# Kernel tuning notes

Hardware: AMD Instinct MI355X
Metric: run time of the kernel (lower is better)

Reference implementation:

```python
import jax, jax.numpy as jnp
import numpy as np

B, NW, L, D = 32, 64, 49, 192
HEADS, PROJ = 8, 256
HD = PROJ // HEADS  # 32


def setup_inputs() -> dict:
    key = jax.random.key(0)
    ks = jax.random.split(key, 12)
    s = 0.02
    return {
        "query": jax.random.normal(ks[0], (B, NW, L, D), jnp.float32),
        "key_": jax.random.normal(ks[1], (B, NW, L, D), jnp.float32),
        "value": jax.random.normal(ks[2], (B, NW, L, D), jnp.float32),
        "mask": jax.random.randint(ks[3], (1, NW, 1, L, L), 0, 2).astype(bool),
        "Wq": jax.random.normal(ks[4], (D, PROJ), jnp.float32) * s,
        "bq": jnp.zeros((PROJ,), jnp.float32),
        "Wk": jax.random.normal(ks[5], (D, PROJ), jnp.float32) * s,
        "bk": jnp.zeros((PROJ,), jnp.float32),
        "Wv": jax.random.normal(ks[6], (D, PROJ), jnp.float32) * s,
        "Ww": jax.random.normal(ks[7], (PROJ, D), jnp.float32) * s,
        "bw": jnp.zeros((D,), jnp.float32),
    }


def reference(query, key_, value, mask, Wq, bq, Wk, bk, Wv, Ww, bw):
    scale = 1.0 / (HD ** 0.5)
    # projections, split heads: [B, NW, L, PROJ] -> [B, NW, H, L, HD]
    def split_heads(x):
        return x.reshape(B, NW, L, HEADS, HD).transpose(0, 1, 3, 2, 4)

    q = split_heads(query @ Wq + bq)
    k = split_heads(key_ @ Wk + bk)
    v = split_heads(value @ Wv)  # no bias, matching proj_v

    # scores: [B, NW, H, L, L]
    scores = jnp.einsum("bwhnc,bwhmc->bwhnm", q, k) * scale
    scores = jnp.where(mask, jnp.float32(-1000.0), scores)
    attn = jax.nn.softmax(scores, axis=-1)
    # dropout inactive: training=False and enable_sampling=False

    out = jnp.einsum("bwhnm,bwhmc->bwhnc", attn, v)
    out = out.transpose(0, 1, 3, 2, 4).reshape(B, NW, L, PROJ)
    out = out @ Ww + bw
    return out
```

## Files before the change

### kernel.cpp

```cpp
#include <hip/hip_runtime.h>

#define B_    32
#define NW_   64
#define BW_   2048
#define L_    49
#define D_    192
#define PROJ_ 256
#define H_    8
#define HD_   32

typedef __attribute__((ext_vector_type(8))) short bf16x8;
typedef __attribute__((ext_vector_type(4))) float f32x4;

#define QK_OFF    24576
#define LDS_BYTES 78848

__device__ __forceinline__ short f2bf(float f) {
    union { float f; unsigned u; } v; v.f = f;
    unsigned r = v.u + 0x7FFFu + ((v.u >> 16) & 1u);
    return (short)(r >> 16);
}

__device__ __forceinline__ unsigned cvtpk(float lo, float hi) {
    unsigned r;
    asm("v_cvt_pk_bf16_f32 %0, %1, %2" : "=v"(r) : "v"(lo), "v"(hi));
    return r;
}

__global__ __launch_bounds__(256) void prep_kernel(
    const float* __restrict__ Wq, const float* __restrict__ Wk,
    const float* __restrict__ Wv, const float* __restrict__ Ww,
    const int* __restrict__ mask,
    short* __restrict__ Wqt, short* __restrict__ Wkt,
    short* __restrict__ Wvt, short* __restrict__ Wwt,
    unsigned long long* __restrict__ mbits)
{
    const int b   = blockIdx.x;
    const int tid = threadIdx.x;
    if (b < 768) {
        const int sel = b >> 8, n = b & 255;
        const float* src = (sel == 0) ? Wq : (sel == 1) ? Wk : Wv;
        short* dst = (sel == 0) ? Wqt : (sel == 1) ? Wkt : Wvt;
        if (tid < D_) dst[n * D_ + tid] = f2bf(src[tid * PROJ_ + n]);
    } else if (b < 960) {
        const int n = b - 768;
        Wwt[n * PROJ_ + tid] = f2bf(Ww[tid * D_ + n]);
    } else {
        const int m = b - 960;
        const int w = m >> 2, chunk = m & 3;
        const int wave = tid >> 6, lane = tid & 63;
        #pragma unroll
        for (int k = 0; k < 4; ++k) {
            const int q = chunk * 16 + wave * 4 + k;
            int val = 0;
            if (q < L_ && lane < L_) val = mask[w * (L_ * L_) + q * L_ + lane];
            unsigned long long bits = __ballot(val != 0);
            if (lane == 0) mbits[w * 64 + q] = bits;
        }
    }
}

__global__ __launch_bounds__(256, 2) void fused_kernel(
    const float* __restrict__ query, const float* __restrict__ key_,
    const float* __restrict__ value,
    const short* __restrict__ Wqt, const short* __restrict__ Wkt,
    const short* __restrict__ Wvt,
    const float* __restrict__ bq, const float* __restrict__ bk,
    const unsigned long long* __restrict__ mbits,
    const short* __restrict__ Wwt, const float* __restrict__ bwb,
    float* __restrict__ out)
{
    extern __shared__ char lds[];

    const int bw   = blockIdx.x;
    const int w    = bw & (NW_ - 1);
    const int tid  = threadIdx.x;
    const int wave = tid >> 6;
    const int lane = tid & 63;
    const int m16  = lane & 15;
    const int quad = lane >> 4;

    const int swz2 = ((m16 >> 1) & 3) << 4;
    const int swz3 = (m16 & 7) << 4;

    char* qkR  = lds + QK_OFF;
    char* slot = lds + wave * 4096;

    unsigned long long mb[4];
    #pragma unroll
    for (int nt = 0; nt < 4; ++nt) mb[nt] = mbits[w * 64 + nt * 16 + m16];

    uint2 vpk[2][4];

    #pragma unroll
    for (int sel = 0; sel < 3; ++sel) {
        const float* x  = (sel == 0) ? query : (sel == 1) ? key_ : value;
        const short* Wt = (sel == 0) ? Wqt : (sel == 1) ? Wkt : Wvt;

        __syncthreads();
        #pragma unroll
        for (int it = 0; it < 12; ++it) {
            const int i = tid + it * 256;
            const int l = i / 48, c4 = i - l * 48;
            uint2 u = {0u, 0u};
            if (l < L_) {
                float4 v = *(const float4*)&x[((size_t)bw * L_ + l) * D_ + c4 * 4];
                u.x = cvtpk(v.x, v.y); u.y = cvtpk(v.z, v.w);
            }
            *(uint2*)(lds + l * 384 + ((c4 * 8) ^ ((l & 7) << 4))) = u;
        }
        __syncthreads();

        f32x4 acc[4][4];
        #pragma unroll
        for (int mt = 0; mt < 4; ++mt)
            #pragma unroll
            for (int nt = 0; nt < 4; ++nt)
                acc[mt][nt] = (f32x4){0.f, 0.f, 0.f, 0.f};

        #pragma unroll
        for (int kc = 0; kc < 6; ++kc) {
            bf16x8 af[4], bfr[4];
            #pragma unroll
            for (int mt = 0; mt < 4; ++mt)
                af[mt] = *(const bf16x8*)(lds + (mt * 16 + m16) * 384 +
                                          ((kc * 64 + quad * 16) ^ swz3));
            #pragma unroll
            for (int nt = 0; nt < 4; ++nt)
                bfr[nt] = *(const bf16x8*)&Wt[(size_t)(wave * 64 + nt * 16 + m16) * D_ +
                                              kc * 32 + quad * 8];
            __builtin_amdgcn_s_setprio(1);
            #pragma unroll
            for (int mt = 0; mt < 4; ++mt)
                #pragma unroll
                for (int nt = 0; nt < 4; ++nt)
                    acc[mt][nt] = __builtin_amdgcn_mfma_f32_16x16x32_bf16(
                        af[mt], bfr[nt], acc[mt][nt], 0, 0, 0);
            __builtin_amdgcn_s_setprio(0);
        }

        if (sel == 2) __syncthreads();

        if (sel < 2) {
            const float* bsel = (sel == 0) ? bq : bk;
            #pragma unroll
            for (int nt = 0; nt < 4; ++nt) {
                const int head = wave * 2 + (nt >> 1);
                const int c = (nt & 1) * 16 + m16;
                const float bias = bsel[wave * 64 + nt * 16 + m16];
                char* db = qkR + head * 6272 + sel * 3136;
                #pragma unroll
                for (int mt = 0; mt < 4; ++mt)
                    #pragma unroll
                    for (int r = 0; r < 4; ++r) {
                        const int i = mt * 16 + quad * 4 + r;
                        if (i < L_)
                            *(short*)(db + i * 64 + ((2 * c) ^ (((i >> 1) & 3) << 4))) =
                                f2bf(acc[mt][nt][r] + bias);
                    }
            }
        } else {
            #pragma unroll
            for (int nt = 0; nt < 4; ++nt) {
                const int c = (nt & 1) * 16 + m16;
                #pragma unroll
                for (int mt = 0; mt < 4; ++mt) {
                    uint2 p;
                    p.x = cvtpk(acc[mt][nt][0], acc[mt][nt][1]);
                    p.y = cvtpk(acc[mt][nt][2], acc[mt][nt][3]);
                    if (nt < 2)
                        *(uint2*)(slot + c * 128 + ((mt * 32 + quad * 8) ^ swz3)) = p;
                    else
                        vpk[nt - 2][mt] = p;
                }
            }
        }
    }

    const float scale = 0.17677669529663687f;

    #pragma unroll 1
    for (int hh = 0; hh < 2; ++hh) {
        const int head = wave * 2 + hh;
        char* qb = qkR + head * 6272;
        char* kb = qb + 3136;

        f32x4 sacc[4][4];
        #pragma unroll
        for (int mt = 0; mt < 4; ++mt)
            #pragma unroll
            for (int nt = 0; nt < 4; ++nt)
                sacc[mt][nt] = (f32x4){0.f, 0.f, 0.f, 0.f};
        {
            bf16x8 kf[4], qf[4];
            #pragma unroll
            for (int mt = 0; mt < 4; ++mt)
                kf[mt] = *(const bf16x8*)(kb + (mt * 16 + m16) * 64 + ((quad * 16) ^ swz2));
            #pragma unroll
            for (int nt = 0; nt < 4; ++nt)
                qf[nt] = *(const bf16x8*)(qb + (nt * 16 + m16) * 64 + ((quad * 16) ^ swz2));
            __builtin_amdgcn_s_setprio(1);
            #pragma unroll
            for (int mt = 0; mt < 4; ++mt)
                #pragma unroll
                for (int nt = 0; nt < 4; ++nt)
                    sacc[mt][nt] = __builtin_amdgcn_mfma_f32_16x16x32_bf16(
                        kf[mt], qf[nt], sacc[mt][nt], 0, 0, 0);
            __builtin_amdgcn_s_setprio(0);
        }

        #pragma unroll
        for (int nt = 0; nt < 4; ++nt) {
            float e[4][4];
            float mx = -1e30f;
            #pragma unroll
            for (int mt = 0; mt < 4; ++mt)
                #pragma unroll
                for (int r = 0; r < 4; ++r) {
                    const int k = mt * 16 + quad * 4 + r;
                    float v = sacc[mt][nt][r] * scale;
                    if (k >= L_) v = -INFINITY;
                    else if ((mb[nt] >> k) & 1ull) v = -1000.0f;
                    e[mt][r] = v;
                    mx = fmaxf(mx, v);
                }
            mx = fmaxf(mx, __shfl_xor(mx, 16, 64));
            mx = fmaxf(mx, __shfl_xor(mx, 32, 64));
            float sum = 0.f;
            #pragma unroll
            for (int mt = 0; mt < 4; ++mt)
                #pragma unroll
                for (int r = 0; r < 4; ++r) {
                    const float ev = __expf(e[mt][r] - mx);
                    e[mt][r] = ev;
                    sum += ev;
                }
            sum += __shfl_xor(sum, 16, 64);
            sum += __shfl_xor(sum, 32, 64);
            const float inv = 1.0f / sum;
            const int prow = nt * 16 + m16;
            if (prow < L_) {
                #pragma unroll
                for (int mt = 0; mt < 4; ++mt) {
                    uint2 p;
                    p.x = cvtpk(e[mt][0] * inv, e[mt][1] * inv);
                    p.y = cvtpk(e[mt][2] * inv, e[mt][3] * inv);
                    *(uint2*)(qb + prow * 128 + ((mt * 32 + quad * 8) ^ swz3)) = p;
                }
            }
        }

        f32x4 oacc[2][4];
        #pragma unroll
        for (int mt2 = 0; mt2 < 2; ++mt2)
            #pragma unroll
            for (int nt = 0; nt < 4; ++nt)
                oacc[mt2][nt] = (f32x4){0.f, 0.f, 0.f, 0.f};
        #pragma unroll
        for (int kc = 0; kc < 2; ++kc) {
            bf16x8 vf[2], pf[4];
            #pragma unroll
            for (int mt2 = 0; mt2 < 2; ++mt2)
                vf[mt2] = *(const bf16x8*)(slot + (mt2 * 16 + m16) * 128 +
                                           ((kc * 64 + quad * 16) ^ swz3));
            #pragma unroll
            for (int nt = 0; nt < 4; ++nt)
                pf[nt] = *(const bf16x8*)(qb + (nt * 16 + m16) * 128 +
                                          ((kc * 64 + quad * 16) ^ swz3));
            __builtin_amdgcn_s_setprio(1);
            #pragma unroll
            for (int mt2 = 0; mt2 < 2; ++mt2)
                #pragma unroll
                for (int nt = 0; nt < 4; ++nt)
                    oacc[mt2][nt] = __builtin_amdgcn_mfma_f32_16x16x32_bf16(
                        vf[mt2], pf[nt], oacc[mt2][nt], 0, 0, 0);
            __builtin_amdgcn_s_setprio(0);
        }

        #pragma unroll
        for (int nt = 0; nt < 4; ++nt) {
            const int prow = nt * 16 + m16;
            if (prow < L_) {
                #pragma unroll
                for (int mt2 = 0; mt2 < 2; ++mt2) {
                    uint2 o;
                    o.x = cvtpk(oacc[mt2][nt][0], oacc[mt2][nt][1]);
                    o.y = cvtpk(oacc[mt2][nt][2], oacc[mt2][nt][3]);
                    *(uint2*)(qb + prow * 64 +
                              ((mt2 * 32 + quad * 8) ^ (((prow >> 1) & 3) << 4))) = o;
                }
            }
        }

        if (hh == 0) {
            #pragma unroll
            for (int nt2 = 0; nt2 < 2; ++nt2) {
                const int c = nt2 * 16 + m16;
                #pragma unroll
                for (int mt = 0; mt < 4; ++mt)
                    *(uint2*)(slot + c * 128 + ((mt * 32 + quad * 8) ^ swz3)) = vpk[nt2][mt];
            }
        }
    }

    __syncthreads();

    f32x4 cacc[4][3];
    #pragma unroll
    for (int mt = 0; mt < 4; ++mt)
        #pragma unroll
        for (int nt = 0; nt < 3; ++nt)
            cacc[mt][nt] = (f32x4){0.f, 0.f, 0.f, 0.f};
    #pragma unroll
    for (int kc = 0; kc < 8; ++kc) {
        char* Oh = qkR + kc * 6272;
        bf16x8 af[4], bfw[3];
        #pragma unroll
        for (int mt = 0; mt < 4; ++mt)
            af[mt] = *(const bf16x8*)(Oh + (mt * 16 + m16) * 64 + ((quad * 16) ^ swz2));
        #pragma unroll
        for (int nt = 0; nt < 3; ++nt)
            bfw[nt] = *(const bf16x8*)&Wwt[(size_t)(wave * 48 + nt * 16 + m16) * PROJ_ +
                                           kc * 32 + quad * 8];
        __builtin_amdgcn_s_setprio(1);
        #pragma unroll
        for (int mt = 0; mt < 4; ++mt)
            #pragma unroll
            for (int nt = 0; nt < 3; ++nt)
                cacc[mt][nt] = __builtin_amdgcn_mfma_f32_16x16x32_bf16(
                    af[mt], bfw[nt], cacc[mt][nt], 0, 0, 0);
        __builtin_amdgcn_s_setprio(0);
    }
    #pragma unroll
    for (int nt = 0; nt < 3; ++nt) {
        const int col = wave * 48 + nt * 16 + m16;
        const float bias = bwb[col];
        #pragma unroll
        for (int mt = 0; mt < 4; ++mt)
            #pragma unroll
            for (int r = 0; r < 4; ++r) {
                const int i = mt * 16 + quad * 4 + r;
                if (i < L_)
                    out[((size_t)bw * L_ + i) * D_ + col] = cacc[mt][nt][r] + bias;
            }
    }
}

extern "C" void kernel_launch(void* const* d_in, const int* in_sizes, int n_in,
                              void* d_out, int out_size, void* d_ws, size_t ws_size,
                              hipStream_t stream) {
    const float* query = (const float*)d_in[0];
    const float* key_  = (const float*)d_in[1];
    const float* value = (const float*)d_in[2];
    const int*   mask  = (const int*)d_in[3];
    const float* Wq    = (const float*)d_in[4];
    const float* bq    = (const float*)d_in[5];
    const float* Wk    = (const float*)d_in[6];
    const float* bk    = (const float*)d_in[7];
    const float* Wv    = (const float*)d_in[8];
    const float* Ww    = (const float*)d_in[9];
    const float* bw    = (const float*)d_in[10];
    float* out = (float*)d_out;

    unsigned long long* mbits = (unsigned long long*)d_ws;
    short* Wqt = (short*)(mbits + 64 * 64);
    short* Wkt = Wqt + PROJ_ * D_;
    short* Wvt = Wkt + PROJ_ * D_;
    short* Wwt = Wvt + PROJ_ * D_;

    static bool attr_set = false;
    if (!attr_set) {
        (void)hipFuncSetAttribute(reinterpret_cast<const void*>(fused_kernel),
                                  hipFuncAttributeMaxDynamicSharedMemorySize, LDS_BYTES);
        attr_set = true;
    }

    prep_kernel<<<dim3(1216), 256, 0, stream>>>(Wq, Wk, Wv, Ww, mask,
                                                Wqt, Wkt, Wvt, Wwt, mbits);
    fused_kernel<<<dim3(BW_), 256, LDS_BYTES, stream>>>(
        query, key_, value, Wqt, Wkt, Wvt, bq, bk, mbits, Wwt, bw, out);
}
```

Before: 367.0 us.

## Use 8 waves per block with one head per wave and in-kernel mask bits

Doubles the block to 512 threads so each wave owns a single attention head instead of two. The Q/K/V projection and output-projection work is split across twice as many waves, and V staging is compacted to make room. Mask bit-packing moves from the prep kernel into the fused kernel's LDS, removing the mbits workspace. This trades more waves per block and higher register pressure under launch_bounds(512,4), and adds a per-block mask read, against shorter serial per-wave work and more latency hiding.

```diff
diff --git a/kernel.cpp b/kernel.cpp
--- a/kernel.cpp
+++ b/kernel.cpp
@@ -13,7 +13,8 @@
 typedef __attribute__((ext_vector_type(4))) float f32x4;
 
 #define QK_OFF    24576
-#define LDS_BYTES 78848
+#define MROW_OFF  74752
+#define LDS_BYTES 76800
 
 __device__ __forceinline__ short f2bf(float f) {
     union { float f; unsigned u; } v; v.f = f;
@@ -27,13 +28,11 @@
     return r;
 }
 
-__global__ __launch_bounds__(256) void prep_kernel(
+__global__ __launch_bounds__(256) void prep_weights(
     const float* __restrict__ Wq, const float* __restrict__ Wk,
     const float* __restrict__ Wv, const float* __restrict__ Ww,
-    const int* __restrict__ mask,
     short* __restrict__ Wqt, short* __restrict__ Wkt,
-    short* __restrict__ Wvt, short* __restrict__ Wwt,
-    unsigned long long* __restrict__ mbits)
+    short* __restrict__ Wvt, short* __restrict__ Wwt)
 {
     const int b   = blockIdx.x;
     const int tid = threadIdx.x;
@@ -42,31 +41,19 @@
         const float* src = (sel == 0) ? Wq : (sel == 1) ? Wk : Wv;
         short* dst = (sel == 0) ? Wqt : (sel == 1) ? Wkt : Wvt;
         if (tid < D_) dst[n * D_ + tid] = f2bf(src[tid * PROJ_ + n]);
-    } else if (b < 960) {
+    } else {
         const int n = b - 768;
         Wwt[n * PROJ_ + tid] = f2bf(Ww[tid * D_ + n]);
-    } else {
-        const int m = b - 960;
-        const int w = m >> 2, chunk = m & 3;
-        const int wave = tid >> 6, lane = tid & 63;
-        #pragma unroll
-        for (int k = 0; k < 4; ++k) {
-            const int q = chunk * 16 + wave * 4 + k;
-            int val = 0;
-            if (q < L_ && lane < L_) val = mask[w * (L_ * L_) + q * L_ + lane];
-            unsigned long long bits = __ballot(val != 0);
-            if (lane == 0) mbits[w * 64 + q] = bits;
-        }
-    }
-}
-
-__global__ __launch_bounds__(256, 2) void fused_kernel(
+    }
+}
+
+__global__ __launch_bounds__(512, 4) void fused_kernel(
     const float* __restrict__ query, const float* __restrict__ key_,
     const float* __restrict__ value,
     const short* __restrict__ Wqt, const short* __restrict__ Wkt,
     const short* __restrict__ Wvt,
     const float* __restrict__ bq, const float* __restrict__ bk,
-    const unsigned long long* __restrict__ mbits,
+    const int* __restrict__ mask,
     const short* __restrict__ Wwt, const float* __restrict__ bwb,
     float* __restrict__ out)
 {
@@ -83,12 +70,10 @@
     const int swz2 = ((m16 >> 1) & 3) << 4;
     const int swz3 = (m16 & 7) << 4;
 
-    char* qkR  = lds + QK_OFF;
-    char* slot = lds + wave * 4096;
-
-    unsigned long long mb[4];
-    #pragma unroll
-    for (int nt = 0; nt < 4; ++nt) mb[nt] = mbits[w * 64 + nt * 16 + m16];
+    char* qb = lds + QK_OFF + wave * 6272;
+    char* kb = qb + 3136;
+    char* vslot = lds + wave * 2560;
+    unsigned long long* mrow = (unsigned long long*)(lds + MROW_OFF);
 
     uint2 vpk[2][4];
 
@@ -99,8 +84,8 @@
 
         __syncthreads();
         #pragma unroll
-        for (int it = 0; it < 12; ++it) {
-            const int i = tid + it * 256;
+        for (int it = 0; it < 6; ++it) {
+            const int i = tid + it * 512;
             const int l = i / 48, c4 = i - l * 48;
             uint2 u = {0u, 0u};
             if (l < L_) {
@@ -109,46 +94,54 @@
             }
             *(uint2*)(lds + l * 384 + ((c4 * 8) ^ ((l & 7) << 4))) = u;
         }
+        if (sel == 0) {
+            #pragma unroll
+            for (int rr = 0; rr < 8; ++rr) {
+                const int row = wave * 8 + rr;
+                int val = 0;
+                if (row < L_ && lane < L_)
+                    val = mask[w * (L_ * L_) + row * L_ + lane];
+                unsigned long long bits = __ballot(val != 0);
+                if (lane == 0) mrow[row] = bits;
+            }
+        }
         __syncthreads();
 
-        f32x4 acc[4][4];
-        #pragma unroll
-        for (int mt = 0; mt < 4; ++mt)
-            #pragma unroll
-            for (int nt = 0; nt < 4; ++nt)
+        f32x4 acc[4][2];
+        #pragma unroll
+        for (int mt = 0; mt < 4; ++mt)
+            #pragma unroll
+            for (int nt = 0; nt < 2; ++nt)
                 acc[mt][nt] = (f32x4){0.f, 0.f, 0.f, 0.f};
 
         #pragma unroll
         for (int kc = 0; kc < 6; ++kc) {
-            bf16x8 af[4], bfr[4];
+            bf16x8 af[4], bfr[2];
             #pragma unroll
             for (int mt = 0; mt < 4; ++mt)
                 af[mt] = *(const bf16x8*)(lds + (mt * 16 + m16) * 384 +
                                           ((kc * 64 + quad * 16) ^ swz3));
             #pragma unroll
-            for (int nt = 0; nt < 4; ++nt)
-                bfr[nt] = *(const bf16x8*)&Wt[(size_t)(wave * 64 + nt * 16 + m16) * D_ +
+            for (int nt = 0; nt < 2; ++nt)
+                bfr[nt] = *(const bf16x8*)&Wt[(size_t)(wave * 32 + nt * 16 + m16) * D_ +
                                               kc * 32 + quad * 8];
             __builtin_amdgcn_s_setprio(1);
             #pragma unroll
             for (int mt = 0; mt < 4; ++mt)
                 #pragma unroll
-                for (int nt = 0; nt < 4; ++nt)
+                for (int nt = 0; nt < 2; ++nt)
                     acc[mt][nt] = __builtin_amdgcn_mfma_f32_16x16x32_bf16(
                         af[mt], bfr[nt], acc[mt][nt], 0, 0, 0);
             __builtin_amdgcn_s_setprio(0);
         }
 
-        if (sel == 2) __syncthreads();
-
         if (sel < 2) {
             const float* bsel = (sel == 0) ? bq : bk;
-            #pragma unroll
-            for (int nt = 0; nt < 4; ++nt) {
-                const int head = wave * 2 + (nt >> 1);
-                const int c = (nt & 1) * 16 + m16;
-                const float bias = bsel[wave * 64 + nt * 16 + m16];
-                char* db = qkR + head * 6272 + sel * 3136;
+            char* db = (sel == 0) ? qb : kb;
+            #pragma unroll
+            for (int nt = 0; nt < 2; ++nt) {
+                const int c = nt * 16 + m16;
+                const float bias = bsel[wave * 32 + c];
                 #pragma unroll
                 for (int mt = 0; mt < 4; ++mt)
                     #pragma unroll
@@ -161,188 +154,188 @@
             }
         } else {
             #pragma unroll
-            for (int nt = 0; nt < 4; ++nt) {
-                const int c = (nt & 1) * 16 + m16;
+            for (int nt = 0; nt < 2; ++nt)
                 #pragma unroll
                 for (int mt = 0; mt < 4; ++mt) {
-                    uint2 p;
-                    p.x = cvtpk(acc[mt][nt][0], acc[mt][nt][1]);
-                    p.y = cvtpk(acc[mt][nt][2], acc[mt][nt][3]);
-                    if (nt < 2)
-                        *(uint2*)(slot + c * 128 + ((mt * 32 + quad * 8) ^ swz3)) = p;
-                    else
-                        vpk[nt - 2][mt] = p;
+                    vpk[nt][mt].x = cvtpk(acc[mt][nt][0], acc[mt][nt][1]);
+                    vpk[nt][mt].y = cvtpk(acc[mt][nt][2], acc[mt][nt][3]);
                 }
-            }
-        }
-    }
+        }
+    }
+
+    __syncthreads();
+
+    #pragma unroll
+    for (int nt = 0; nt < 2; ++nt)
+        #pragma unroll
+        for (int mt = 0; mt < 2; ++mt)
+            *(uint2*)(vslot + (nt * 16 + m16) * 80 + mt * 32 + quad * 8) = vpk[nt][mt];
+
+    unsigned long long mb[4];
+    #pragma unroll
+    for (int nt = 0; nt < 4; ++nt) mb[nt] = mrow[nt * 16 + m16];
 
     const float scale = 0.17677669529663687f;
 
-    #pragma unroll 1
-    for (int hh = 0; hh < 2; ++hh) {
-        const int head = wave * 2 + hh;
-        char* qb = qkR + head * 6272;
-        char* kb = qb + 3136;
-
-        f32x4 sacc[4][4];
+    f32x4 sacc[4][4];
+    #pragma unroll
+    for (int mt = 0; mt < 4; ++mt)
+        #pragma unroll
+        for (int nt = 0; nt < 4; ++nt)
+            sacc[mt][nt] = (f32x4){0.f, 0.f, 0.f, 0.f};
+    {
+        bf16x8 kf[4], qf[4];
+        #pragma unroll
+        for (int mt = 0; mt < 4; ++mt)
+            kf[mt] = *(const bf16x8*)(kb + (mt * 16 + m16) * 64 + ((quad * 16) ^ swz2));
+        #pragma unroll
+        for (int nt = 0; nt < 4; ++nt)
+            qf[nt] = *(const bf16x8*)(qb + (nt * 16 + m16) * 64 + ((quad * 16) ^ swz2));
+        __builtin_amdgcn_s_setprio(1);
         #pragma unroll
         for (int mt = 0; mt < 4; ++mt)
             #pragma unroll
             for (int nt = 0; nt < 4; ++nt)
-                sacc[mt][nt] = (f32x4){0.f, 0.f, 0.f, 0.f};
-        {
-            bf16x8 kf[4], qf[4];
+                sacc[mt][nt] = __builtin_amdgcn_mfma_f32_16x16x32_bf16(
+                    kf[mt], qf[nt], sacc[mt][nt], 0, 0, 0);
+        __builtin_amdgcn_s_setprio(0);
+    }
+
+    #pragma unroll
+    for (int nt = 0; nt < 4; ++nt) {
+        float e[4][4];
+        float mx = -1e30f;
+        #pragma unroll
+        for (int mt = 0; mt < 4; ++mt)
+            #pragma unroll
+            for (int r = 0; r < 4; ++r) {
+                const int k = mt * 16 + quad * 4 + r;
+                float v = sacc[mt][nt][r] * scale;
+                if (k >= L_) v = -INFINITY;
+                else if ((mb[nt] >> k) & 1ull) v = -1000.0f;
+                e[mt][r] = v;
+                mx = fmaxf(mx, v);
+            }
+        mx = fmaxf(mx, __shfl_xor(mx, 16, 64));
+        mx = fmaxf(mx, __shfl_xor(mx, 32, 64));
+        float sum = 0.f;
+        #pragma unroll
+        for (int mt = 0; mt < 4; ++mt)
+            #pragma unroll
+            for (int r = 0; r < 4; ++r) {
+                const float ev = __expf(e[mt][r] - mx);
+                e[mt][r] = ev;
+                sum += ev;
+            }
+        sum += __shfl_xor(sum, 16, 64);
+        sum += __shfl_xor(sum, 32, 64);
+        const float inv = 1.0f / sum;
+        const int prow = nt * 16 + m16;
+        if (prow < L_) {
+            #pragma unroll
+            for (int mt = 0; mt < 4; ++mt) {
+                uint2 p;
+                p.x = cvtpk(e[mt][0] * inv, e[mt][1] * inv);
+                p.y = cvtpk(e[mt][2] * inv, e[mt][3] * inv);
+                *(uint2*)(qb + prow * 128 + ((mt * 32 + quad * 8) ^ swz3)) = p;
+            }
+        }
+    }
+
+    f32x4 oacc[2][4];
+    #pragma unroll
+    for (int mt2 = 0; mt2 < 2; ++mt2)
+        #pragma unroll
+        for (int nt = 0; nt < 4; ++nt)
+            oacc[mt2][nt] = (f32x4){0.f, 0.f, 0.f, 0.f};
+    #pragma unroll
+    for (int kc = 0; kc < 2; ++kc) {
+        bf16x8 vf[2], pf[4];
+        #pragma unroll
+        for (int mt2 = 0; mt2 < 2; ++mt2)
+            vf[mt2] = *(const bf16x8*)(vslot + (mt2 * 16 + m16) * 80 + quad * 16);
+        #pragma unroll
+        for (int nt = 0; nt < 4; ++nt)
+            pf[nt] = *(const bf16x8*)(qb + (nt * 16 + m16) * 128 +
+                                      ((kc * 64 + quad * 16) ^ swz3));
+        __builtin_amdgcn_s_setprio(1);
+        #pragma unroll
+        for (int mt2 = 0; mt2 < 2; ++mt2)
+            #pragma unroll
+            for (int nt = 0; nt < 4; ++nt)
+                oacc[mt2][nt] = __builtin_amdgcn_mfma_f32_16x16x32_bf16(
+                    vf[mt2], pf[nt], oacc[mt2][nt], 0, 0, 0);
+        __builtin_amdgcn_s_setprio(0);
+        if (kc == 0) {
+            #pragma unroll
+            for (int nt = 0; nt < 2; ++nt)
+                #pragma unroll
+                for (int mt = 2; mt < 4; ++mt)
+                    *(uint2*)(vslot + (nt * 16 + m16) * 80 + (mt - 2) * 32 + quad * 8) =
+                        vpk[nt][mt];
+        }
+    }
+
+    #pragma unroll
+    for (int nt = 0; nt < 4; ++nt) {
+        const int prow = nt * 16 + m16;
+        if (prow < L_) {
+            #pragma unroll
+            for (int mt2 = 0; mt2 < 2; ++mt2) {
+                uint2 o;
+                o.x = cvtpk(oacc[mt2][nt][0], oacc[mt2][nt][1]);
+                o.y = cvtpk(oacc[mt2][nt][2], oacc[mt2][nt][3]);
+                *(uint2*)(qb + prow * 64 +
+                          ((mt2 * 32 + quad * 8) ^ (((prow >> 1) & 3) << 4))) = o;
+            }
+        }
+    }
+
+    __syncthreads();
+
+    f32x4 cacc[4][2];
+    #pragma unroll
+    for (int mt = 0; mt < 4; ++mt)
+        #pragma unroll
+        for (int nt = 0; nt < 2; ++nt)
+            cacc[mt][nt] = (f32x4){0.f, 0.f, 0.f, 0.f};
+    #pragma unroll
+    for (int kc = 0; kc < 8; ++kc) {
+        char* Oh = lds + QK_OFF + kc * 6272;
+        bf16x8 af[4], bfw[2];
+        #pragma unroll
+        for (int mt = 0; mt < 4; ++mt)
+            af[mt] = *(const bf16x8*)(Oh + (mt * 16 + m16) * 64 + ((quad * 16) ^ swz2));
+        bfw[0] = *(const bf16x8*)&Wwt[(size_t)(wave * 16 + m16) * PROJ_ +
+                                      kc * 32 + quad * 8];
+        if (wave < 4)
+            bfw[1] = *(const bf16x8*)&Wwt[(size_t)(128 + wave * 16 + m16) * PROJ_ +
+                                          kc * 32 + quad * 8];
+        __builtin_amdgcn_s_setprio(1);
+        #pragma unroll
+        for (int mt = 0; mt < 4; ++mt) {
+            cacc[mt][0] = __builtin_amdgcn_mfma_f32_16x16x32_bf16(
+                af[mt], bfw[0], cacc[mt][0], 0, 0, 0);
+            if (wave < 4)
+                cacc[mt][1] = __builtin_amdgcn_mfma_f32_16x16x32_bf16(
+                    af[mt], bfw[1], cacc[mt][1], 0, 0, 0);
+        }
+        __builtin_amdgcn_s_setprio(0);
+    }
+    #pragma unroll
+    for (int nt = 0; nt < 2; ++nt) {
+        if (nt == 0 || wave < 4) {
+            const int col = nt * 128 + wave * 16 + m16;
+            const float bias = bwb[col];
             #pragma unroll
             for (int mt = 0; mt < 4; ++mt)
-                kf[mt] = *(const bf16x8*)(kb + (mt * 16 + m16) * 64 + ((quad * 16) ^ swz2));
-            #pragma unroll
-            for (int nt = 0; nt < 4; ++nt)
-                qf[nt] = *(const bf16x8*)(qb + (nt * 16 + m16) * 64 + ((quad * 16) ^ swz2));
-            __builtin_amdgcn_s_setprio(1);
-            #pragma unroll
-            for (int mt = 0; mt < 4; ++mt)
-                #pragma unroll
-                for (int nt = 0; nt < 4; ++nt)
-                    sacc[mt][nt] = __builtin_amdgcn_mfma_f32_16x16x32_bf16(
-                        kf[mt], qf[nt], sacc[mt][nt], 0, 0, 0);
-            __builtin_amdgcn_s_setprio(0);
-        }
-
-        #pragma unroll
-        for (int nt = 0; nt < 4; ++nt) {
-            float e[4][4];
-            float mx = -1e30f;
-            #pragma unroll
-            for (int mt = 0; mt < 4; ++mt)
                 #pragma unroll
                 for (int r = 0; r < 4; ++r) {
-                    const int k = mt * 16 + quad * 4 + r;
-                    float v = sacc[mt][nt][r] * scale;
-                    if (k >= L_) v = -INFINITY;
-                    else if ((mb[nt] >> k) & 1ull) v = -1000.0f;
-                    e[mt][r] = v;
-                    mx = fmaxf(mx, v);
+                    const int i = mt * 16 + quad * 4 + r;
+                    if (i < L_)
+                        out[((size_t)bw * L_ + i) * D_ + col] = cacc[mt][nt][r] + bias;
                 }
-            mx = fmaxf(mx, __shfl_xor(mx, 16, 64));
-            mx = fmaxf(mx, __shfl_xor(mx, 32, 64));
-            float sum = 0.f;
-            #pragma unroll
-            for (int mt = 0; mt < 4; ++mt)
-                #pragma unroll
-                for (int r = 0; r < 4; ++r) {
-                    const float ev = __expf(e[mt][r] - mx);
-                    e[mt][r] = ev;
-                    sum += ev;
-                }
-            sum += __shfl_xor(sum, 16, 64);
-            sum += __shfl_xor(sum, 32, 64);
-            const float inv = 1.0f / sum;
-            const int prow = nt * 16 + m16;
-            if (prow < L_) {
-                #pragma unroll
-                for (int mt = 0; mt < 4; ++mt) {
-                    uint2 p;
-                    p.x = cvtpk(e[mt][0] * inv, e[mt][1] * inv);
-                    p.y = cvtpk(e[mt][2] * inv, e[mt][3] * inv);
-                    *(uint2*)(qb + prow * 128 + ((mt * 32 + quad * 8) ^ swz3)) = p;
-                }
-            }
-        }
-
-        f32x4 oacc[2][4];
-        #pragma unroll
-        for (int mt2 = 0; mt2 < 2; ++mt2)
-            #pragma unroll
-            for (int nt = 0; nt < 4; ++nt)
-                oacc[mt2][nt] = (f32x4){0.f, 0.f, 0.f, 0.f};
-        #pragma unroll
-        for (int kc = 0; kc < 2; ++kc) {
-            bf16x8 vf[2], pf[4];
-            #pragma unroll
-            for (int mt2 = 0; mt2 < 2; ++mt2)
-                vf[mt2] = *(const bf16x8*)(slot + (mt2 * 16 + m16) * 128 +
-                                           ((kc * 64 + quad * 16) ^ swz3));
-            #pragma unroll
-            for (int nt = 0; nt < 4; ++nt)
-                pf[nt] = *(const bf16x8*)(qb + (nt * 16 + m16) * 128 +
-                                          ((kc * 64 + quad * 16) ^ swz3));
-            __builtin_amdgcn_s_setprio(1);
-            #pragma unroll
-            for (int mt2 = 0; mt2 < 2; ++mt2)
-                #pragma unroll
-                for (int nt = 0; nt < 4; ++nt)
-                    oacc[mt2][nt] = __builtin_amdgcn_mfma_f32_16x16x32_bf16(
-                        vf[mt2], pf[nt], oacc[mt2][nt], 0, 0, 0);
-            __builtin_amdgcn_s_setprio(0);
-        }
-
-        #pragma unroll
-        for (int nt = 0; nt < 4; ++nt) {
-            const int prow = nt * 16 + m16;
-            if (prow < L_) {
-                #pragma unroll
-                for (int mt2 = 0; mt2 < 2; ++mt2) {
-                    uint2 o;
-                    o.x = cvtpk(oacc[mt2][nt][0], oacc[mt2][nt][1]);
-                    o.y = cvtpk(oacc[mt2][nt][2], oacc[mt2][nt][3]);
-                    *(uint2*)(qb + prow * 64 +
-                              ((mt2 * 32 + quad * 8) ^ (((prow >> 1) & 3) << 4))) = o;
-                }
-            }
-        }
-
-        if (hh == 0) {
-            #pragma unroll
-            for (int nt2 = 0; nt2 < 2; ++nt2) {
-                const int c = nt2 * 16 + m16;
-                #pragma unroll
-                for (int mt = 0; mt < 4; ++mt)
-                    *(uint2*)(slot + c * 128 + ((mt * 32 + quad * 8) ^ swz3)) = vpk[nt2][mt];
-            }
-        }
-    }
-
-    __syncthreads();
-
-    f32x4 cacc[4][3];
-    #pragma unroll
-    for (int mt = 0; mt < 4; ++mt)
-        #pragma unroll
-        for (int nt = 0; nt < 3; ++nt)
-            cacc[mt][nt] = (f32x4){0.f, 0.f, 0.f, 0.f};
-    #pragma unroll
-    for (int kc = 0; kc < 8; ++kc) {
-        char* Oh = qkR + kc * 6272;
-        bf16x8 af[4], bfw[3];
-        #pragma unroll
-        for (int mt = 0; mt < 4; ++mt)
-            af[mt] = *(const bf16x8*)(Oh + (mt * 16 + m16) * 64 + ((quad * 16) ^ swz2));
-        #pragma unroll
-        for (int nt = 0; nt < 3; ++nt)
-            bfw[nt] = *(const bf16x8*)&Wwt[(size_t)(wave * 48 + nt * 16 + m16) * PROJ_ +
-                                           kc * 32 + quad * 8];
-        __builtin_amdgcn_s_setprio(1);
-        #pragma unroll
-        for (int mt = 0; mt < 4; ++mt)
-            #pragma unroll
-            for (int nt = 0; nt < 3; ++nt)
-                cacc[mt][nt] = __builtin_amdgcn_mfma_f32_16x16x32_bf16(
-                    af[mt], bfw[nt], cacc[mt][nt], 0, 0, 0);
-        __builtin_amdgcn_s_setprio(0);
-    }
-    #pragma unroll
-    for (int nt = 0; nt < 3; ++nt) {
-        const int col = wave * 48 + nt * 16 + m16;
-        const float bias = bwb[col];
-        #pragma unroll
-        for (int mt = 0; mt < 4; ++mt)
-            #pragma unroll
-            for (int r = 0; r < 4; ++r) {
-                const int i = mt * 16 + quad * 4 + r;
-                if (i < L_)
-                    out[((size_t)bw * L_ + i) * D_ + col] = cacc[mt][nt][r] + bias;
-            }
+        }
     }
 }
 
@@ -362,8 +355,7 @@
     const float* bw    = (const float*)d_in[10];
     float* out = (float*)d_out;
 
-    unsigned long long* mbits = (unsigned long long*)d_ws;
-    short* Wqt = (short*)(mbits + 64 * 64);
+    short* Wqt = (short*)d_ws;
     short* Wkt = Wqt + PROJ_ * D_;
     short* Wvt = Wkt + PROJ_ * D_;
     short* Wwt = Wvt + PROJ_ * D_;
@@ -375,8 +367,7 @@
         attr_set = true;
     }
 
-    prep_kernel<<<dim3(1216), 256, 0, stream>>>(Wq, Wk, Wv, Ww, mask,
-                                                Wqt, Wkt, Wvt, Wwt, mbits);
-    fused_kernel<<<dim3(BW_), 256, LDS_BYTES, stream>>>(
-        query, key_, value, Wqt, Wkt, Wvt, bq, bk, mbits, Wwt, bw, out);
-}
+    prep_weights<<<dim3(960), 256, 0, stream>>>(Wq, Wk, Wv, Ww, Wqt, Wkt, Wvt, Wwt);
+    fused_kernel<<<dim3(BW_), 512, LDS_BYTES, stream>>>(
+        query, key_, value, Wqt, Wkt, Wvt, bq, bk, mask, Wwt, bw, out);
+}
```

After: 410.4 us. 1.12x slower.
